# Performance work log

Hardware: AMD Instinct MI355X
Metric: run time of the kernel (lower is better)

## Reference

```python
import jax, jax.numpy as jnp
import numpy as np

ETA = 0.01
SCALE = 0.05  # feature scale so exp(-sqdist) stays in fp32 range


def _sqdist(a, b):
    # squared euclidean distances == torch.cdist(a, b) ** 2, shape [len(a), len(b)]
    return jnp.maximum(
        jnp.sum(a * a, axis=1)[:, None] + jnp.sum(b * b, axis=1)[None, :] - 2.0 * (a @ b.T),
        0.0,
    )


def setup_inputs() -> dict:
    key = jax.random.key(0)
    ks = jax.random.split(key, 16)
    N, B, D, DY, L = 20000, 2048, 64, 32, 100
    x = jax.random.normal(ks[0], (B, D), dtype=jnp.float32) * SCALE
    star_features = jax.random.normal(ks[1], (N, D), dtype=jnp.float32) * SCALE
    star_labels = jax.random.normal(ks[2], (N, DY), dtype=jnp.float32)
    features1 = jax.random.normal(ks[3], (N, D), dtype=jnp.float32) * SCALE
    features2 = jax.random.normal(ks[4], (N, D), dtype=jnp.float32) * SCALE
    labels_unique1 = jax.random.normal(ks[5], (L, DY), dtype=jnp.float32)
    labels_unique2 = jax.random.normal(ks[6], (L, DY), dtype=jnp.float32)
    label_distances1 = jax.random.uniform(ks[7], (L, L), dtype=jnp.float32)
    label_distances2 = jax.random.uniform(ks[8], (L, L), dtype=jnp.float32)
    W1 = jax.random.normal(ks[9], (D, DY), dtype=jnp.float32) / np.float32(np.sqrt(D))
    b1 = jax.random.normal(ks[10], (DY,), dtype=jnp.float32) * 0.01
    W2 = jax.random.normal(ks[11], (D, DY), dtype=jnp.float32) / np.float32(np.sqrt(D))
    b2 = jax.random.normal(ks[12], (DY,), dtype=jnp.float32) * 0.01
    label_indices1 = jax.random.randint(ks[13], (N,), 0, L)
    label_indices2 = jax.random.randint(ks[14], (N,), 0, L)
    return {
        "x": x, "star_features": star_features, "star_labels": star_labels,
        "features1": features1, "features2": features2,
        "labels_unique1": labels_unique1, "labels_unique2": labels_unique2,
        "label_distances1": label_distances1, "label_distances2": label_distances2,
        "W1": W1, "b1": b1, "W2": W2, "b2": b2,
        "label_indices1": label_indices1, "label_indices2": label_indices2,
    }


def _forward(x, star_features, star_labels, features1, features2,
             labels_unique1, labels_unique2, label_distances1, label_distances2,
             W1, b1, W2, b2, label_indices1, label_indices2):
    B = x.shape[0]
    # --- exact-match search against dataset_star (torch.eq(...).all(2).nonzero()) ---
    # sqdist == 0 <=> rows identical; gives [B, N] mask without a [B, N, D] broadcast
    d0 = _sqdist(x, star_features)
    mask = d0 <= 0.0
    has_match = jnp.any(mask, axis=1)              # [B]
    match_idx = jnp.argmax(mask, axis=1)           # first matching star index per query

    # star->x Nadaraya-Watson kernel, shared by both dataset branches
    e_star = jnp.exp(-_sqdist(star_features, x))   # [N, B]
    e_star_sum = jnp.sum(e_star, axis=0)           # [B]

    def branch(feats, W, bvec, uniq, lidx, ldist):
        xt_un = ((feats.T @ e_star) / e_star_sum).T          # [B, D]
        xt = jnp.where(has_match[:, None], feats[match_idx], xt_un)
        # model forward (linear classifier) + project_labels (cdist + argmin)
        y = xt @ W + bvec                                     # [B, DY]
        y_idx = jnp.argmin(_sqdist(y, uniq), axis=1)          # [B]
        # transport_labels, method='all_samples'
        ld = ldist[lidx][:, y_idx]                            # [N, B]
        e2 = jnp.exp(-_sqdist(feats, xt) - ETA * ld)          # [N, B]
        return ((star_labels.T @ e2) / jnp.sum(e2, axis=0)).T  # [B, DY]

    y1 = branch(features1, W1, b1, labels_unique1, label_indices1, label_distances1)
    y2 = branch(features2, W2, b2, labels_unique2, label_indices2, label_distances2)
    return (y1 + y2) * 0.5


def reference(x, star_features, star_labels, features1, features2,
              labels_unique1, labels_unique2, label_distances1, label_distances2,
              W1, b1, W2, b2, label_indices1, label_indices2):
    return _forward(x, star_features, star_labels, features1, features2,
                    labels_unique1, labels_unique2, label_distances1, label_distances2,
                    W1, b1, W2, b2, label_indices1, label_indices2)
```

## Files before the change

kernel.cpp:

```cpp
#include <hip/hip_runtime.h>
#include <cstddef>

#define NQ 2048
#define NS 20000
#define NSP 20032
#define DD 64
#define DY 32
#define LL 100
#define NT 313
#define PSTR 72
#define LOG2E 1.4426950408889634f
#define NELD (-0.01f * 1.4426950408889634f)

typedef __attribute__((ext_vector_type(8))) short bfrag;
typedef __attribute__((ext_vector_type(4))) float ffrag;

#if __has_builtin(__builtin_amdgcn_exp2f)
#define EXP2(x) __builtin_amdgcn_exp2f(x)
#else
#define EXP2(x) exp2f(x)
#endif

#define MFMA __builtin_amdgcn_mfma_f32_16x16x32_bf16

#define GLOAD_LDS(gp, lp)                                                       \
  __builtin_amdgcn_global_load_lds(                                             \
      (const __attribute__((address_space(1))) unsigned int*)(gp),              \
      (__attribute__((address_space(3))) unsigned int*)(lp), 16, 0, 0)

__device__ __forceinline__ unsigned short bf16rne(float v) {
  unsigned int u = __float_as_uint(v);
  u += 0x7FFFu + ((u >> 16) & 1u);
  return (unsigned short)(u >> 16);
}

__device__ __forceinline__ uint4 pack8(const unsigned short* o) {
  uint4 q;
  q.x = (unsigned int)o[0] | ((unsigned int)o[1] << 16);
  q.y = (unsigned int)o[2] | ((unsigned int)o[3] << 16);
  q.z = (unsigned int)o[4] | ((unsigned int)o[5] << 16);
  q.w = (unsigned int)o[6] | ((unsigned int)o[7] << 16);
  return q;
}

__global__ __launch_bounds__(256) void k_prep(
    const float* __restrict__ star, const float* __restrict__ f1,
    const float* __restrict__ f2, const float* __restrict__ slab,
    const float* __restrict__ x,
    const int* __restrict__ lidx1, const int* __restrict__ lidx2,
    unsigned short* __restrict__ star_b, unsigned short* __restrict__ f1_rm,
    unsigned short* __restrict__ f2_rm, unsigned short* __restrict__ vt1,
    unsigned short* __restrict__ vt2, unsigned short* __restrict__ xb,
    float* __restrict__ nsl, float* __restrict__ nf1l, float* __restrict__ nf2l,
    float* __restrict__ nxl, int* __restrict__ lidxp1, int* __restrict__ lidxp2,
    int* __restrict__ matchIdx)
{
  __shared__ float tile[64][65];
  const int tid = threadIdx.x;
  if (blockIdx.x >= NT) {
    int b = (blockIdx.x - NT) * 256 + tid;
    if (b >= NQ) return;
    const float* px = x + (size_t)b * DD;
    float s = 0.f;
    for (int d = 0; d < DD; d += 4) {
      float4 v = *(const float4*)(px + d);
      s += v.x*v.x + v.y*v.y + v.z*v.z + v.w*v.w;
      unsigned int lo = (unsigned int)bf16rne(v.x * (2.f * LOG2E)) |
                        ((unsigned int)bf16rne(v.y * (2.f * LOG2E)) << 16);
      unsigned int hi = (unsigned int)bf16rne(v.z * (2.f * LOG2E)) |
                        ((unsigned int)bf16rne(v.w * (2.f * LOG2E)) << 16);
      *(uint2*)(xb + (size_t)b * DD + d) = make_uint2(lo, hi);
    }
    nxl[b] = LOG2E * s;
    matchIdx[b] = NS;
    return;
  }
  const int i0 = blockIdx.x * 64;
  const int r = tid >> 2, cs = (tid & 3) * 16;
  const int dT = tid >> 2, is = (tid & 3) * 16;
  const bool okr = (i0 + r) < NS;

  const float* srcs[3] = {star, f1, f2};
  unsigned short* dsts[3] = {star_b, f1_rm, f2_rm};
  float* norms[3] = {nsl, nf1l, nf2l};
#pragma unroll 1
  for (int a = 0; a < 3; a++) {
    float v[16];
    const float* src = srcs[a] + (size_t)(i0 + r) * DD + cs;
#pragma unroll
    for (int q = 0; q < 4; q++) {
      float4 t4 = okr ? *(const float4*)(src + q * 4) : make_float4(0.f, 0.f, 0.f, 0.f);
      v[4*q+0] = t4.x; v[4*q+1] = t4.y; v[4*q+2] = t4.z; v[4*q+3] = t4.w;
    }
    unsigned short ob[16];
#pragma unroll
    for (int j = 0; j < 16; j++) { ob[j] = bf16rne(v[j]); tile[r][cs + j] = v[j]; }
    *(uint4*)(dsts[a] + (size_t)(i0 + r) * DD + cs) = pack8(ob);
    *(uint4*)(dsts[a] + (size_t)(i0 + r) * DD + cs + 8) = pack8(ob + 8);
    __syncthreads();
    if (tid < 64) {
      float s = 0.f;
      for (int d = 0; d < DD; d++) s += tile[tid][d] * tile[tid][d];
      norms[a][i0 + tid] = (i0 + tid) < NS ? LOG2E * s : 1e30f;
    }
    if (a > 0) {
      unsigned short tb[16];
#pragma unroll
      for (int j = 0; j < 16; j++) tb[j] = bf16rne(tile[is + j][dT]);
      unsigned short* dst = vt1 + (size_t)((a - 1) * DD + dT) * NSP + i0 + is;
      *(uint4*)dst = pack8(tb);
      *(uint4*)(dst + 8) = pack8(tb + 8);
    }
    __syncthreads();
  }

  if (tid < 128) {
    const int r2 = tid >> 1, cs2 = (tid & 1) * 16;
    const bool ok2 = (i0 + r2) < NS;
    const float* src = slab + (size_t)(i0 + r2) * DY + cs2;
#pragma unroll
    for (int q = 0; q < 4; q++) {
      float4 t4 = ok2 ? *(const float4*)(src + q * 4) : make_float4(0.f, 0.f, 0.f, 0.f);
      tile[r2][cs2+4*q+0] = t4.x; tile[r2][cs2+4*q+1] = t4.y;
      tile[r2][cs2+4*q+2] = t4.z; tile[r2][cs2+4*q+3] = t4.w;
    }
  }
  __syncthreads();
  if (tid < 128) {
    const int d2 = tid >> 2, is2 = (tid & 3) * 16;
    unsigned short tb[16];
#pragma unroll
    for (int j = 0; j < 16; j++) tb[j] = bf16rne(tile[is2 + j][d2]);
    unsigned short* dst = vt2 + (size_t)d2 * NSP + i0 + is2;
    *(uint4*)dst = pack8(tb);
    *(uint4*)(dst + 8) = pack8(tb + 8);
  }
  if (tid < 64) {
    int i = i0 + tid;
    bool ok = i < NS;
    lidxp1[i] = ok ? lidx1[i] : 0;
    lidxp2[i] = ok ? lidx2[i] : 0;
  }
}

__global__ __launch_bounds__(256, 3) void k_star(
    const unsigned short* __restrict__ xb, const unsigned short* __restrict__ star_b,
    const unsigned short* __restrict__ vt1, const float* __restrict__ nsl,
    const float* __restrict__ nxl,
    float* __restrict__ xtp, float* __restrict__ sump,
    int* __restrict__ matchIdx, int nch)
{
  __shared__ __align__(16) unsigned short sm[4096 + 8192 + 4 * 32 * PSTR];
  unsigned short* aT = sm;
  unsigned short* vT = sm + 4096;
  const int tid = threadIdx.x;
  const int w = tid >> 6, lane = tid & 63;
  const int col = lane & 15, quad = lane >> 4;
  const int x0s = quad ^ (col & 7);
  const int x1s = x0s ^ 4;
  unsigned short* myp = sm + 4096 + 8192 + w * (32 * PSTR);
  const int b0 = blockIdx.x * 128 + w * 32;
  const int k = blockIdx.y;
  const int t0 = (k * NT) / nch, t1 = ((k + 1) * NT) / nch;

  bfrag xq00 = *(const bfrag*)(xb + (size_t)(b0 + col) * DD + quad * 8);
  bfrag xq01 = *(const bfrag*)(xb + (size_t)(b0 + col) * DD + 32 + quad * 8);
  bfrag xq10 = *(const bfrag*)(xb + (size_t)(b0 + 16 + col) * DD + quad * 8);
  bfrag xq11 = *(const bfrag*)(xb + (size_t)(b0 + 16 + col) * DD + 32 + quad * 8);
  const float nx0 = nxl[b0 + col], nx1 = nxl[b0 + 16 + col];

  ffrag acc[8][2];
#pragma unroll
  for (int n = 0; n < 8; n++) {
    acc[n][0] = (ffrag){0.f, 0.f, 0.f, 0.f};
    acc[n][1] = (ffrag){0.f, 0.f, 0.f, 0.f};
  }
  float es0 = 0.f, es1 = 0.f;
  int lmin0 = NS, lmin1 = NS;

  for (int t = t0; t < t1; ++t) {
    const int i0 = t * 64;
#pragma unroll
    for (int j = 0; j < 2; j++) {
      int S = ((w * 2 + j) << 6) + lane;
      int r = S >> 3, cs = S & 7;
      GLOAD_LDS(star_b + (size_t)(i0 + r) * DD + ((cs ^ (r & 7)) << 3),
                aT + ((w * 2 + j) << 9));
    }
#pragma unroll
    for (int j = 0; j < 4; j++) {
      int S = ((w * 4 + j) << 6) + lane;
      int r = S >> 3, cs = S & 7;
      GLOAD_LDS(vt1 + (size_t)r * NSP + i0 + ((cs ^ (r & 7)) << 3),
                vT + ((w * 4 + j) << 9));
    }
    __syncthreads();
#pragma unroll
    for (int m = 0; m < 4; m++) {
      const int row = m * 16 + col;
      bfrag a0 = *(const bfrag*)(aT + row * 64 + x0s * 8);
      bfrag a1 = *(const bfrag*)(aT + row * 64 + x1s * 8);
      ffrag c0 = (ffrag){0.f, 0.f, 0.f, 0.f};
      ffrag c1 = (ffrag){0.f, 0.f, 0.f, 0.f};
      c0 = MFMA(a0, xq00, c0, 0, 0, 0); c0 = MFMA(a1, xq01, c0, 0, 0, 0);
      c1 = MFMA(a0, xq10, c1, 0, 0, 0); c1 = MFMA(a1, xq11, c1, 0, 0, 0);
      float4 nsv = *(const float4*)(nsl + i0 + m * 16 + quad * 4);
      float nsa[4] = {nsv.x, nsv.y, nsv.z, nsv.w};
      const int ibase = i0 + m * 16 + quad * 4;
      unsigned short p0[4], p1[4];
#pragma unroll
      for (int r = 0; r < 4; r++) {
        float g0 = c0[r] - nsa[r];
        float g1 = c1[r] - nsa[r];
        if (g0 >= nx0) lmin0 = min(lmin0, ibase + r);
        if (g1 >= nx1) lmin1 = min(lmin1, ibase + r);
        float e0 = EXP2(g0), e1 = EXP2(g1);
        es0 += e0; es1 += e1;
        p0[r] = bf16rne(e0); p1[r] = bf16rne(e1);
      }
      *(uint2*)(myp + col * PSTR + m * 16 + quad * 4) =
          make_uint2((unsigned)p0[0] | ((unsigned)p0[1] << 16),
                     (unsigned)p0[2] | ((unsigned)p0[3] << 16));
      *(uint2*)(myp + (col + 16) * PSTR + m * 16 + quad * 4) =
          make_uint2((unsigned)p1[0] | ((unsigned)p1[1] << 16),
                     (unsigned)p1[2] | ((unsigned)p1[3] << 16));
    }
    bfrag pa0 = *(const bfrag*)(myp + col * PSTR + quad * 8);
    bfrag pa1 = *(const bfrag*)(myp + col * PSTR + 32 + quad * 8);
    bfrag pb0 = *(const bfrag*)(myp + (col + 16) * PSTR + quad * 8);
    bfrag pb1 = *(const bfrag*)(myp + (col + 16) * PSTR + 32 + quad * 8);
#pragma unroll
    for (int n = 0; n < 8; n++) {
      const int row = n * 16 + col;
      bfrag v0 = *(const bfrag*)(vT + row * 64 + x0s * 8);
      bfrag v1 = *(const bfrag*)(vT + row * 64 + x1s * 8);
      acc[n][0] = MFMA(pa0, v0, acc[n][0], 0, 0, 0);
      acc[n][0] = MFMA(pa1, v1, acc[n][0], 0, 0, 0);
      acc[n][1] = MFMA(pb0, v0, acc[n][1], 0, 0, 0);
      acc[n][1] = MFMA(pb1, v1, acc[n][1], 0, 0, 0);
    }
    __syncthreads();
  }

#pragma unroll
  for (int h = 0; h < 2; h++)
#pragma unroll
    for (int n = 0; n < 8; n++)
#pragma unroll
      for (int r = 0; r < 4; r++) {
        int b = b0 + h * 16 + quad * 4 + r;
        xtp[((size_t)k * NQ + b) * 128 + n * 16 + col] = acc[n][h][r];
      }
  es0 += __shfl_xor(es0, 16, 64); es0 += __shfl_xor(es0, 32, 64);
  es1 += __shfl_xor(es1, 16, 64); es1 += __shfl_xor(es1, 32, 64);
  if (quad == 0) {
    sump[(size_t)k * NQ + b0 + col] = es0;
    sump[(size_t)k * NQ + b0 + 16 + col] = es1;
  }
  if (lmin0 < NS) atomicMin(matchIdx + b0 + col, lmin0);
  if (lmin1 < NS) atomicMin(matchIdx + b0 + 16 + col, lmin1);
}

__global__ __launch_bounds__(256) void k_mid(
    const float* __restrict__ xtp, const float* __restrict__ sump,
    const int* __restrict__ matchIdx,
    const float* __restrict__ f1, const float* __restrict__ f2,
    const float* __restrict__ W1, const float* __restrict__ b1,
    const float* __restrict__ W2, const float* __restrict__ b2,
    const float* __restrict__ u1, const float* __restrict__ u2,
    const float* __restrict__ ld1, const float* __restrict__ ld2,
    unsigned short* __restrict__ xtb1, unsigned short* __restrict__ xtb2,
    int* __restrict__ yid1, int* __restrict__ yid2,
    float* __restrict__ lgP1f, float* __restrict__ lgP2f, int nch)
{
  __shared__ float xts[2][4][64];
  __shared__ float ys[4][64];
  __shared__ int yids[2][4];
  const int lane = threadIdx.x & 63;
  const int w = __builtin_amdgcn_readfirstlane(threadIdx.x >> 6);
  const int b = blockIdx.x * 4 + w;

  float s1 = 0.f, s2 = 0.f, S = 0.f;
  for (int kk = 0; kk < nch; kk++) {
    const float* row = xtp + ((size_t)kk * NQ + b) * 128;
    s1 += row[lane];
    s2 += row[64 + lane];
    S  += sump[(size_t)kk * NQ + b];
  }
  const int m = matchIdx[b];
  float xa, xb_;
  if (m < NS) {
    xa = f1[(size_t)m * DD + lane];
    xb_ = f2[(size_t)m * DD + lane];
  } else {
    xa = s1 / S;
    xb_ = s2 / S;
  }
  xtb1[(size_t)b * DD + lane] = bf16rne(xa * (2.f * LOG2E));
  xtb2[(size_t)b * DD + lane] = bf16rne(xb_ * (2.f * LOG2E));
  xts[0][w][lane] = xa;
  xts[1][w][lane] = xb_;
  __syncthreads();

  const int half = lane >> 5;
  const int j = lane & 31;
  const float* W = half ? W2 : W1;
  float y = (half ? b2 : b1)[j];
  for (int d = 0; d < DD; d++) y += xts[half][w][d] * W[d * DY + j];
  ys[w][lane] = y;
  __syncthreads();

#pragma unroll
  for (int p = 0; p < 2; p++) {
    const float* u = p ? u2 : u1;
    unsigned long long best = ~0ull;
#pragma unroll
    for (int h = 0; h < 2; h++) {
      int l = lane + h * 64;
      if (l < LL) {
        float dist = 0.f;
        for (int jj = 0; jj < DY; jj++) {
          float diff = ys[w][p * 32 + jj] - u[(size_t)l * DY + jj];
          dist += diff * diff;
        }
        unsigned long long pk = ((unsigned long long)__float_as_uint(dist) << 32) | (unsigned)l;
        best = best < pk ? best : pk;
      }
    }
#pragma unroll
    for (int off = 32; off > 0; off >>= 1) {
      unsigned long long o = __shfl_xor(best, off, 64);
      best = best < o ? best : o;
    }
    if (lane == 0) {
      int yy = (int)(best & 0xffffffffull);
      (p ? yid2 : yid1)[b] = yy;
      yids[p][w] = yy;
    }
  }
  __syncthreads();
  for (int idx = threadIdx.x; idx < 2 * LL * 4; idx += 256) {
    int p = idx >= LL * 4;
    int rem = idx - p * LL * 4;
    int l = rem >> 2, w2 = rem & 3;
    int bq = blockIdx.x * 4 + w2;
    float val = NELD * (p ? ld2 : ld1)[l * LL + yids[p][w2]];
    int bb = bq >> 5, c = bq & 15, hf = (bq >> 4) & 1;
    (p ? lgP2f : lgP1f)[(((size_t)l * 64 + bb) * 16 + c) * 2 + hf] = val;
  }
}

__global__ __launch_bounds__(256, 4) void k_out(
    const unsigned short* __restrict__ xtb1, const unsigned short* __restrict__ xtb2,
    const unsigned short* __restrict__ f1_rm, const unsigned short* __restrict__ f2_rm,
    const unsigned short* __restrict__ vt2,
    const float* __restrict__ nf1l, const float* __restrict__ nf2l,
    const int* __restrict__ lidxp1, const int* __restrict__ lidxp2,
    const float2* __restrict__ lgP1, const float2* __restrict__ lgP2,
    float* __restrict__ qp1, float* __restrict__ qp2,
    float* __restrict__ qsp1, float* __restrict__ qsp2, int nch)
{
  __shared__ __align__(16) unsigned short sm[4096 + 2048 + 4 * 32 * PSTR];
  unsigned short* aT = sm;
  unsigned short* vT = sm + 4096;
  const int br = blockIdx.z;
  const unsigned short* xtb = br ? xtb2 : xtb1;
  const unsigned short* f_rm = br ? f2_rm : f1_rm;
  const float* nfl = br ? nf2l : nf1l;
  const int* lidxp = br ? lidxp2 : lidxp1;
  const float2* lgP = br ? lgP2 : lgP1;
  float* qp = br ? qp2 : qp1;
  float* qsp = br ? qsp2 : qsp1;

  const int tid = threadIdx.x;
  const int w = tid >> 6, lane = tid & 63;
  const int col = lane & 15, quad = lane >> 4;
  const int x0s = quad ^ (col & 7);
  const int x1s = x0s ^ 4;
  unsigned short* myp = sm + 4096 + 2048 + w * (32 * PSTR);
  const int b0 = blockIdx.x * 128 + w * 32;
  const int bb = blockIdx.x * 4 + w;
  const int k = blockIdx.y;
  const int t0 = (k * NT) / nch, t1 = ((k + 1) * NT) / nch;

  bfrag xq00 = *(const bfrag*)(xtb + (size_t)(b0 + col) * DD + quad * 8);
  bfrag xq01 = *(const bfrag*)(xtb + (size_t)(b0 + col) * DD + 32 + quad * 8);
  bfrag xq10 = *(const bfrag*)(xtb + (size_t)(b0 + 16 + col) * DD + quad * 8);
  bfrag xq11 = *(const bfrag*)(xtb + (size_t)(b0 + 16 + col) * DD + 32 + quad * 8);

  ffrag acc[2][2];
#pragma unroll
  for (int n = 0; n < 2; n++) {
    acc[n][0] = (ffrag){0.f, 0.f, 0.f, 0.f};
    acc[n][1] = (ffrag){0.f, 0.f, 0.f, 0.f};
  }
  float es0 = 0.f, es1 = 0.f;

  for (int t = t0; t < t1; ++t) {
    const int i0 = t * 64;
#pragma unroll
    for (int j = 0; j < 2; j++) {
      int S = ((w * 2 + j) << 6) + lane;
      int r = S >> 3, cs = S & 7;
      GLOAD_LDS(f_rm + (size_t)(i0 + r) * DD + ((cs ^ (r & 7)) << 3),
                aT + ((w * 2 + j) << 9));
    }
    {
      int S = (w << 6) + lane;
      int r = S >> 3, cs = S & 7;
      GLOAD_LDS(vt2 + (size_t)r * NSP + i0 + ((cs ^ (r & 7)) << 3),
                vT + (w << 9));
    }
    __syncthreads();
#pragma unroll
    for (int m = 0; m < 4; m++) {
      const int row = m * 16 + col;
      int4 lv = *(const int4*)(lidxp + i0 + m * 16 + quad * 4);
      float2 g0v = lgP[((size_t)lv.x * 64 + bb) * 16 + col];
      float2 g1v = lgP[((size_t)lv.y * 64 + bb) * 16 + col];
      float2 g2v = lgP[((size_t)lv.z * 64 + bb) * 16 + col];
      float2 g3v = lgP[((size_t)lv.w * 64 + bb) * 16 + col];
      bfrag a0 = *(const bfrag*)(aT + row * 64 + x0s * 8);
      bfrag a1 = *(const bfrag*)(aT + row * 64 + x1s * 8);
      ffrag c0 = (ffrag){0.f, 0.f, 0.f, 0.f};
      ffrag c1 = (ffrag){0.f, 0.f, 0.f, 0.f};
      c0 = MFMA(a0, xq00, c0, 0, 0, 0); c0 = MFMA(a1, xq01, c0, 0, 0, 0);
      c1 = MFMA(a0, xq10, c1, 0, 0, 0); c1 = MFMA(a1, xq11, c1, 0, 0, 0);
      float4 nfv = *(const float4*)(nfl + i0 + m * 16 + quad * 4);
      float ea0 = EXP2(c0[0] - nfv.x + g0v.x), eb0 = EXP2(c1[0] - nfv.x + g0v.y);
      float ea1 = EXP2(c0[1] - nfv.y + g1v.x), eb1 = EXP2(c1[1] - nfv.y + g1v.y);
      float ea2 = EXP2(c0[2] - nfv.z + g2v.x), eb2 = EXP2(c1[2] - nfv.z + g2v.y);
      float ea3 = EXP2(c0[3] - nfv.w + g3v.x), eb3 = EXP2(c1[3] - nfv.w + g3v.y);
      es0 += ea0 + ea1 + ea2 + ea3;
      es1 += eb0 + eb1 + eb2 + eb3;
      *(uint2*)(myp + col * PSTR + m * 16 + quad * 4) =
          make_uint2((unsigned)bf16rne(ea0) | ((unsigned)bf16rne(ea1) << 16),
                     (unsigned)bf16rne(ea2) | ((unsigned)bf16rne(ea3) << 16));
      *(uint2*)(myp + (col + 16) * PSTR + m * 16 + quad * 4) =
          make_uint2((unsigned)bf16rne(eb0) | ((unsigned)bf16rne(eb1) << 16),
                     (unsigned)bf16rne(eb2) | ((unsigned)bf16rne(eb3) << 16));
    }
    bfrag pa0 = *(const bfrag*)(myp + col * PSTR + quad * 8);
    bfrag pa1 = *(const bfrag*)(myp + col * PSTR + 32 + quad * 8);
    bfrag pb0 = *(const bfrag*)(myp + (col + 16) * PSTR + quad * 8);
    bfrag pb1 = *(const bfrag*)(myp + (col + 16) * PSTR + 32 + quad * 8);
#pragma unroll
    for (int n = 0; n < 2; n++) {
      const int row = n * 16 + col;
      bfrag v0 = *(const bfrag*)(vT + row * 64 + x0s * 8);
      bfrag v1 = *(const bfrag*)(vT + row * 64 + x1s * 8);
      acc[n][0] = MFMA(pa0, v0, acc[n][0], 0, 0, 0);
      acc[n][0] = MFMA(pa1, v1, acc[n][0], 0, 0, 0);
      acc[n][1] = MFMA(pb0, v0, acc[n][1], 0, 0, 0);
      acc[n][1] = MFMA(pb1, v1, acc[n][1], 0, 0, 0);
    }
    __syncthreads();
  }

#pragma unroll
  for (int h = 0; h < 2; h++)
#pragma unroll
    for (int n = 0; n < 2; n++)
#pragma unroll
      for (int r = 0; r < 4; r++) {
        int b = b0 + h * 16 + quad * 4 + r;
        qp[((size_t)k * NQ + b) * DY + n * 16 + col] = acc[n][h][r];
      }
  es0 += __shfl_xor(es0, 16, 64); es0 += __shfl_xor(es0, 32, 64);
  es1 += __shfl_xor(es1, 16, 64); es1 += __shfl_xor(es1, 32, 64);
  if (quad == 0) {
    qsp[(size_t)k * NQ + b0 + col] = es0;
    qsp[(size_t)k * NQ + b0 + 16 + col] = es1;
  }
}

__global__ __launch_bounds__(256) void k_fin(
    const float* __restrict__ qp1, const float* __restrict__ qsp1,
    const float* __restrict__ qp2, const float* __restrict__ qsp2,
    float* __restrict__ out, int nch)
{
  int t = blockIdx.x * 256 + threadIdx.x;
  if (t >= NQ * DY) return;
  int b = t >> 5, j = t & 31;
  float n1 = 0.f, d1 = 0.f, n2 = 0.f, d2 = 0.f;
  for (int kk = 0; kk < nch; kk++) {
    n1 += qp1[((size_t)kk * NQ + b) * DY + j];
    n2 += qp2[((size_t)kk * NQ + b) * DY + j];
    d1 += qsp1[(size_t)kk * NQ + b];
    d2 += qsp2[(size_t)kk * NQ + b];
  }
  out[t] = 0.5f * (n1 / d1 + n2 / d2);
}

extern "C" void kernel_launch(void* const* d_in, const int* in_sizes, int n_in,
                              void* d_out, int out_size, void* d_ws, size_t ws_size,
                              hipStream_t stream)
{
  const float* x    = (const float*)d_in[0];
  const float* star = (const float*)d_in[1];
  const float* slab = (const float*)d_in[2];
  const float* f1   = (const float*)d_in[3];
  const float* f2   = (const float*)d_in[4];
  const float* u1   = (const float*)d_in[5];
  const float* u2   = (const float*)d_in[6];
  const float* ld1  = (const float*)d_in[7];
  const float* ld2  = (const float*)d_in[8];
  const float* W1   = (const float*)d_in[9];
  const float* b1   = (const float*)d_in[10];
  const float* W2   = (const float*)d_in[11];
  const float* b2   = (const float*)d_in[12];
  const int* lidx1  = (const int*)d_in[13];
  const int* lidx2  = (const int*)d_in[14];
  float* out = (float*)d_out;

  auto al = [](size_t b) { return (b + 255) & ~(size_t)255; };
  const size_t auxBytes =
      al((size_t)NQ * DD * 2) +
      3 * al((size_t)NSP * DD * 2) +
      al((size_t)128 * NSP * 2) +
      al((size_t)32 * NSP * 2) +
      2 * al((size_t)NQ * DD * 2) +
      3 * al((size_t)NSP * 4) +
      al((size_t)NQ * 4) +
      2 * al((size_t)LL * 64 * 16 * 8) +
      2 * al((size_t)NSP * 4) +
      3 * al((size_t)NQ * 4);
  const size_t pc1 = (size_t)NQ * 4 * 129;
  const size_t pc2 = (size_t)NQ * 4 * 2 * (DY + 1);
  int nch1 = 48, nch2 = 48;
  while ((nch1 > 6) && auxBytes + nch1 * pc1 + nch2 * pc2 > ws_size) {
    nch1 >>= 1;
    if (nch2 > 6) nch2 >>= 1;
  }

  char* base = (char*)d_ws;
  size_t off = 0;
  auto alloc = [&](size_t bytes) -> char* {
    char* p = base + off;
    off = (off + bytes + 255) & ~(size_t)255;
    return p;
  };
  float* xtp  = (float*)alloc((size_t)nch1 * NQ * 128 * 4);
  float* sump = (float*)alloc((size_t)nch1 * NQ * 4);
  float* qp1  = (float*)alloc((size_t)nch2 * NQ * DY * 4);
  float* qp2  = (float*)alloc((size_t)nch2 * NQ * DY * 4);
  float* qsp1 = (float*)alloc((size_t)nch2 * NQ * 4);
  float* qsp2 = (float*)alloc((size_t)nch2 * NQ * 4);
  unsigned short* xb     = (unsigned short*)alloc((size_t)NQ * DD * 2);
  unsigned short* star_b = (unsigned short*)alloc((size_t)NSP * DD * 2);
  unsigned short* f1_rm  = (unsigned short*)alloc((size_t)NSP * DD * 2);
  unsigned short* f2_rm  = (unsigned short*)alloc((size_t)NSP * DD * 2);
  unsigned short* vt1    = (unsigned short*)alloc((size_t)128 * NSP * 2);
  unsigned short* vt2    = (unsigned short*)alloc((size_t)32 * NSP * 2);
  unsigned short* xtb1   = (unsigned short*)alloc((size_t)NQ * DD * 2);
  unsigned short* xtb2   = (unsigned short*)alloc((size_t)NQ * DD * 2);
  float* nsl   = (float*)alloc(NSP * 4);
  float* nf1l  = (float*)alloc(NSP * 4);
  float* nf2l  = (float*)alloc(NSP * 4);
  float* nxl   = (float*)alloc(NQ * 4);
  float2* lgP1 = (float2*)alloc((size_t)LL * 64 * 16 * 8);
  float2* lgP2 = (float2*)alloc((size_t)LL * 64 * 16 * 8);
  int* lidxp1 = (int*)alloc(NSP * 4);
  int* lidxp2 = (int*)alloc(NSP * 4);
  int* matchIdx = (int*)alloc(NQ * 4);
  int* yid1 = (int*)alloc(NQ * 4);
  int* yid2 = (int*)alloc(NQ * 4);

  k_prep<<<NT + (NQ + 255) / 256, 256, 0, stream>>>(
      star, f1, f2, slab, x, lidx1, lidx2,
      star_b, f1_rm, f2_rm, vt1, vt2, xb,
      nsl, nf1l, nf2l, nxl, lidxp1, lidxp2, matchIdx);

  k_star<<<dim3(NQ / 128, nch1), 256, 0, stream>>>(
      xb, star_b, vt1, nsl, nxl, xtp, sump, matchIdx, nch1);

  k_mid<<<NQ / 4, 256, 0, stream>>>(
      xtp, sump, matchIdx, f1, f2, W1, b1, W2, b2, u1, u2, ld1, ld2,
      xtb1, xtb2, yid1, yid2, (float*)lgP1, (float*)lgP2, nch1);

  k_out<<<dim3(NQ / 128, nch2, 2), 256, 0, stream>>>(
      xtb1, xtb2, f1_rm, f2_rm, vt2, nf1l, nf2l, lidxp1, lidxp2,
      lgP1, lgP2, qp1, qp2, qsp1, qsp2, nch2);

  k_fin<<<(NQ * DY + 255) / 256, 256, 0, stream>>>(qp1, qsp1, qp2, qsp2, out, nch2);
}
```

Before: 227.2 us.

## Parallelize prep over phases, store star partials in bf16, use packed bf16 conversion

The prep kernel moves its three sequential feature passes and the label transpose onto separate grid-y phases, so they run as parallel blocks. Row norms now come from per-thread partial sums instead of a serial 64-wide loop. The star kernel's per-chunk partial outputs are stored as bf16 rather than fp32, halving that workspace traffic, and the float-to-bf16 packing uses the packed hardware conversion intrinsic. The output kernel's chunk count drops from 48 to 40. Storing partials in bf16 adds rounding error before the cross-chunk sum.

```diff
diff --git a/kernel.cpp b/kernel.cpp
--- a/kernel.cpp
+++ b/kernel.cpp
@@ -1,4 +1,5 @@
 #include <hip/hip_runtime.h>
+#include <hip/hip_bf16.h>
 #include <cstddef>
 
 #define NQ 2048
@@ -32,6 +33,13 @@
   unsigned int u = __float_as_uint(v);
   u += 0x7FFFu + ((u >> 16) & 1u);
   return (unsigned short)(u >> 16);
+}
+
+__device__ __forceinline__ unsigned int pk2(float a, float b) {
+  __hip_bfloat162 h = __float22bfloat162_rn(make_float2(a, b));
+  unsigned int u;
+  __builtin_memcpy(&u, &h, 4);
+  return u;
 }
 
 __device__ __forceinline__ uint4 pack8(const unsigned short* o) {
@@ -56,8 +64,11 @@
     int* __restrict__ matchIdx)
 {
   __shared__ float tile[64][65];
+  __shared__ float pn[64][4];
   const int tid = threadIdx.x;
+  const int ph = blockIdx.y;
   if (blockIdx.x >= NT) {
+    if (ph != 0) return;
     int b = (blockIdx.x - NT) * 256 + tid;
     if (b >= NQ) return;
     const float* px = x + (size_t)b * DD;
@@ -65,81 +76,84 @@
     for (int d = 0; d < DD; d += 4) {
       float4 v = *(const float4*)(px + d);
       s += v.x*v.x + v.y*v.y + v.z*v.z + v.w*v.w;
-      unsigned int lo = (unsigned int)bf16rne(v.x * (2.f * LOG2E)) |
-                        ((unsigned int)bf16rne(v.y * (2.f * LOG2E)) << 16);
-      unsigned int hi = (unsigned int)bf16rne(v.z * (2.f * LOG2E)) |
-                        ((unsigned int)bf16rne(v.w * (2.f * LOG2E)) << 16);
-      *(uint2*)(xb + (size_t)b * DD + d) = make_uint2(lo, hi);
+      *(uint2*)(xb + (size_t)b * DD + d) =
+          make_uint2(pk2(v.x * (2.f * LOG2E), v.y * (2.f * LOG2E)),
+                     pk2(v.z * (2.f * LOG2E), v.w * (2.f * LOG2E)));
     }
     nxl[b] = LOG2E * s;
     matchIdx[b] = NS;
     return;
   }
   const int i0 = blockIdx.x * 64;
-  const int r = tid >> 2, cs = (tid & 3) * 16;
-  const int dT = tid >> 2, is = (tid & 3) * 16;
+  const int r = tid >> 2, q = tid & 3, cs = q * 16;
   const bool okr = (i0 + r) < NS;
 
-  const float* srcs[3] = {star, f1, f2};
-  unsigned short* dsts[3] = {star_b, f1_rm, f2_rm};
-  float* norms[3] = {nsl, nf1l, nf2l};
-#pragma unroll 1
-  for (int a = 0; a < 3; a++) {
-    float v[16];
-    const float* src = srcs[a] + (size_t)(i0 + r) * DD + cs;
-#pragma unroll
-    for (int q = 0; q < 4; q++) {
-      float4 t4 = okr ? *(const float4*)(src + q * 4) : make_float4(0.f, 0.f, 0.f, 0.f);
-      v[4*q+0] = t4.x; v[4*q+1] = t4.y; v[4*q+2] = t4.z; v[4*q+3] = t4.w;
-    }
-    unsigned short ob[16];
-#pragma unroll
-    for (int j = 0; j < 16; j++) { ob[j] = bf16rne(v[j]); tile[r][cs + j] = v[j]; }
-    *(uint4*)(dsts[a] + (size_t)(i0 + r) * DD + cs) = pack8(ob);
-    *(uint4*)(dsts[a] + (size_t)(i0 + r) * DD + cs + 8) = pack8(ob + 8);
+  if (ph == 3) {
+    if (tid < 128) {
+      const int r2 = tid >> 1, cs2 = (tid & 1) * 16;
+      const bool ok2 = (i0 + r2) < NS;
+      const float* src = slab + (size_t)(i0 + r2) * DY + cs2;
+#pragma unroll
+      for (int qq = 0; qq < 4; qq++) {
+        float4 t4 = ok2 ? *(const float4*)(src + qq * 4) : make_float4(0.f, 0.f, 0.f, 0.f);
+        tile[r2][cs2+4*qq+0] = t4.x; tile[r2][cs2+4*qq+1] = t4.y;
+        tile[r2][cs2+4*qq+2] = t4.z; tile[r2][cs2+4*qq+3] = t4.w;
+      }
+    }
     __syncthreads();
-    if (tid < 64) {
-      float s = 0.f;
-      for (int d = 0; d < DD; d++) s += tile[tid][d] * tile[tid][d];
-      norms[a][i0 + tid] = (i0 + tid) < NS ? LOG2E * s : 1e30f;
-    }
-    if (a > 0) {
+    if (tid < 128) {
+      const int d2 = tid >> 2, is2 = (tid & 3) * 16;
       unsigned short tb[16];
 #pragma unroll
-      for (int j = 0; j < 16; j++) tb[j] = bf16rne(tile[is + j][dT]);
-      unsigned short* dst = vt1 + (size_t)((a - 1) * DD + dT) * NSP + i0 + is;
+      for (int j = 0; j < 16; j++) tb[j] = bf16rne(tile[is2 + j][d2]);
+      unsigned short* dst = vt2 + (size_t)d2 * NSP + i0 + is2;
       *(uint4*)dst = pack8(tb);
       *(uint4*)(dst + 8) = pack8(tb + 8);
     }
-    __syncthreads();
-  }
-
-  if (tid < 128) {
-    const int r2 = tid >> 1, cs2 = (tid & 1) * 16;
-    const bool ok2 = (i0 + r2) < NS;
-    const float* src = slab + (size_t)(i0 + r2) * DY + cs2;
-#pragma unroll
-    for (int q = 0; q < 4; q++) {
-      float4 t4 = ok2 ? *(const float4*)(src + q * 4) : make_float4(0.f, 0.f, 0.f, 0.f);
-      tile[r2][cs2+4*q+0] = t4.x; tile[r2][cs2+4*q+1] = t4.y;
-      tile[r2][cs2+4*q+2] = t4.z; tile[r2][cs2+4*q+3] = t4.w;
-    }
+    if (tid < 64) {
+      int i = i0 + tid;
+      bool ok = i < NS;
+      lidxp1[i] = ok ? lidx1[i] : 0;
+      lidxp2[i] = ok ? lidx2[i] : 0;
+    }
+    return;
+  }
+
+  const float* src_ = (ph == 0) ? star : (ph == 1) ? f1 : f2;
+  unsigned short* dst_ = (ph == 0) ? star_b : (ph == 1) ? f1_rm : f2_rm;
+  float* norm_ = (ph == 0) ? nsl : (ph == 1) ? nf1l : nf2l;
+
+  float v[16];
+  const float* src = src_ + (size_t)(i0 + r) * DD + cs;
+#pragma unroll
+  for (int qq = 0; qq < 4; qq++) {
+    float4 t4 = okr ? *(const float4*)(src + qq * 4) : make_float4(0.f, 0.f, 0.f, 0.f);
+    v[4*qq+0] = t4.x; v[4*qq+1] = t4.y; v[4*qq+2] = t4.z; v[4*qq+3] = t4.w;
+  }
+  float p = 0.f;
+  unsigned short ob[16];
+#pragma unroll
+  for (int j = 0; j < 16; j++) { p += v[j] * v[j]; ob[j] = bf16rne(v[j]); }
+  pn[r][q] = p;
+  *(uint4*)(dst_ + (size_t)(i0 + r) * DD + cs) = pack8(ob);
+  *(uint4*)(dst_ + (size_t)(i0 + r) * DD + cs + 8) = pack8(ob + 8);
+  if (ph) {
+#pragma unroll
+    for (int j = 0; j < 16; j++) tile[r][cs + j] = v[j];
   }
   __syncthreads();
-  if (tid < 128) {
-    const int d2 = tid >> 2, is2 = (tid & 3) * 16;
+  if (tid < 64) {
+    float s = pn[tid][0] + pn[tid][1] + pn[tid][2] + pn[tid][3];
+    norm_[i0 + tid] = (i0 + tid) < NS ? LOG2E * s : 1e30f;
+  }
+  if (ph) {
+    const int dT = tid >> 2, is = q * 16;
     unsigned short tb[16];
 #pragma unroll
-    for (int j = 0; j < 16; j++) tb[j] = bf16rne(tile[is2 + j][d2]);
-    unsigned short* dst = vt2 + (size_t)d2 * NSP + i0 + is2;
+    for (int j = 0; j < 16; j++) tb[j] = bf16rne(tile[is + j][dT]);
+    unsigned short* dst = vt1 + (size_t)((ph - 1) * DD + dT) * NSP + i0 + is;
     *(uint4*)dst = pack8(tb);
     *(uint4*)(dst + 8) = pack8(tb + 8);
-  }
-  if (tid < 64) {
-    int i = i0 + tid;
-    bool ok = i < NS;
-    lidxp1[i] = ok ? lidx1[i] : 0;
-    lidxp2[i] = ok ? lidx2[i] : 0;
   }
 }
 
@@ -147,7 +161,7 @@
     const unsigned short* __restrict__ xb, const unsigned short* __restrict__ star_b,
     const unsigned short* __restrict__ vt1, const float* __restrict__ nsl,
     const float* __restrict__ nxl,
-    float* __restrict__ xtp, float* __restrict__ sump,
+    unsigned short* __restrict__ xtp, float* __restrict__ sump,
     int* __restrict__ matchIdx, int nch)
 {
   __shared__ __align__(16) unsigned short sm[4096 + 8192 + 4 * 32 * PSTR];
@@ -207,23 +221,20 @@
       float4 nsv = *(const float4*)(nsl + i0 + m * 16 + quad * 4);
       float nsa[4] = {nsv.x, nsv.y, nsv.z, nsv.w};
       const int ibase = i0 + m * 16 + quad * 4;
-      unsigned short p0[4], p1[4];
+      float e0[4], e1[4];
 #pragma unroll
       for (int r = 0; r < 4; r++) {
         float g0 = c0[r] - nsa[r];
         float g1 = c1[r] - nsa[r];
         if (g0 >= nx0) lmin0 = min(lmin0, ibase + r);
         if (g1 >= nx1) lmin1 = min(lmin1, ibase + r);
-        float e0 = EXP2(g0), e1 = EXP2(g1);
-        es0 += e0; es1 += e1;
-        p0[r] = bf16rne(e0); p1[r] = bf16rne(e1);
+        e0[r] = EXP2(g0); e1[r] = EXP2(g1);
+        es0 += e0[r]; es1 += e1[r];
       }
       *(uint2*)(myp + col * PSTR + m * 16 + quad * 4) =
-          make_uint2((unsigned)p0[0] | ((unsigned)p0[1] << 16),
-                     (unsigned)p0[2] | ((unsigned)p0[3] << 16));
+          make_uint2(pk2(e0[0], e0[1]), pk2(e0[2], e0[3]));
       *(uint2*)(myp + (col + 16) * PSTR + m * 16 + quad * 4) =
-          make_uint2((unsigned)p1[0] | ((unsigned)p1[1] << 16),
-                     (unsigned)p1[2] | ((unsigned)p1[3] << 16));
+          make_uint2(pk2(e1[0], e1[1]), pk2(e1[2], e1[3]));
     }
     bfrag pa0 = *(const bfrag*)(myp + col * PSTR + quad * 8);
     bfrag pa1 = *(const bfrag*)(myp + col * PSTR + 32 + quad * 8);
@@ -249,7 +260,7 @@
 #pragma unroll
       for (int r = 0; r < 4; r++) {
         int b = b0 + h * 16 + quad * 4 + r;
-        xtp[((size_t)k * NQ + b) * 128 + n * 16 + col] = acc[n][h][r];
+        xtp[((size_t)k * NQ + b) * 128 + n * 16 + col] = bf16rne(acc[n][h][r]);
       }
   es0 += __shfl_xor(es0, 16, 64); es0 += __shfl_xor(es0, 32, 64);
   es1 += __shfl_xor(es1, 16, 64); es1 += __shfl_xor(es1, 32, 64);
@@ -262,7 +273,7 @@
 }
 
 __global__ __launch_bounds__(256) void k_mid(
-    const float* __restrict__ xtp, const float* __restrict__ sump,
+    const unsigned short* __restrict__ xtp, const float* __restrict__ sump,
     const int* __restrict__ matchIdx,
     const float* __restrict__ f1, const float* __restrict__ f2,
     const float* __restrict__ W1, const float* __restrict__ b1,
@@ -282,9 +293,9 @@
 
   float s1 = 0.f, s2 = 0.f, S = 0.f;
   for (int kk = 0; kk < nch; kk++) {
-    const float* row = xtp + ((size_t)kk * NQ + b) * 128;
-    s1 += row[lane];
-    s2 += row[64 + lane];
+    const unsigned short* row = xtp + ((size_t)kk * NQ + b) * 128;
+    s1 += __uint_as_float((unsigned int)row[lane] << 16);
+    s2 += __uint_as_float((unsigned int)row[64 + lane] << 16);
     S  += sump[(size_t)kk * NQ + b];
   }
   const int m = matchIdx[b];
@@ -434,11 +445,9 @@
       es0 += ea0 + ea1 + ea2 + ea3;
       es1 += eb0 + eb1 + eb2 + eb3;
       *(uint2*)(myp + col * PSTR + m * 16 + quad * 4) =
-          make_uint2((unsigned)bf16rne(ea0) | ((unsigned)bf16rne(ea1) << 16),
-                     (unsigned)bf16rne(ea2) | ((unsigned)bf16rne(ea3) << 16));
+          make_uint2(pk2(ea0, ea1), pk2(ea2, ea3));
       *(uint2*)(myp + (col + 16) * PSTR + m * 16 + quad * 4) =
-          make_uint2((unsigned)bf16rne(eb0) | ((unsigned)bf16rne(eb1) << 16),
-                     (unsigned)bf16rne(eb2) | ((unsigned)bf16rne(eb3) << 16));
+          make_uint2(pk2(eb0, eb1), pk2(eb2, eb3));
     }
     bfrag pa0 = *(const bfrag*)(myp + col * PSTR + quad * 8);
     bfrag pa1 = *(const bfrag*)(myp + col * PSTR + 32 + quad * 8);
@@ -525,12 +534,12 @@
       2 * al((size_t)LL * 64 * 16 * 8) +
       2 * al((size_t)NSP * 4) +
       3 * al((size_t)NQ * 4);
-  const size_t pc1 = (size_t)NQ * 4 * 129;
+  const size_t pc1 = (size_t)NQ * (128 * 2 + 4);
   const size_t pc2 = (size_t)NQ * 4 * 2 * (DY + 1);
-  int nch1 = 48, nch2 = 48;
+  int nch1 = 48, nch2 = 40;
   while ((nch1 > 6) && auxBytes + nch1 * pc1 + nch2 * pc2 > ws_size) {
     nch1 >>= 1;
-    if (nch2 > 6) nch2 >>= 1;
+    nch2 >>= 1;
   }
 
   char* base = (char*)d_ws;
@@ -540,7 +549,7 @@
     off = (off + bytes + 255) & ~(size_t)255;
     return p;
   };
-  float* xtp  = (float*)alloc((size_t)nch1 * NQ * 128 * 4);
+  unsigned short* xtp = (unsigned short*)alloc((size_t)nch1 * NQ * 128 * 2);
   float* sump = (float*)alloc((size_t)nch1 * NQ * 4);
   float* qp1  = (float*)alloc((size_t)nch2 * NQ * DY * 4);
   float* qp2  = (float*)alloc((size_t)nch2 * NQ * DY * 4);
@@ -566,7 +575,7 @@
   int* yid1 = (int*)alloc(NQ * 4);
   int* yid2 = (int*)alloc(NQ * 4);
 
-  k_prep<<<NT + (NQ + 255) / 256, 256, 0, stream>>>(
+  k_prep<<<dim3(NT + (NQ + 255) / 256, 4), 256, 0, stream>>>(
       star, f1, f2, slab, x, lidx1, lidx2,
       star_b, f1_rm, f2_rm, vt1, vt2, xb,
       nsl, nf1l, nf2l, nxl, lidxp1, lidxp2, matchIdx);
```

Result: slower. 285.0 us (+25.4%).
